# Kernel optimization log

Measured on AMD Instinct MI355X. Metric: run time of the kernel, lower is better.

Reference implementation:

```python
import jax, jax.numpy as jnp
import numpy as np
from math import pi

B, CIN, COUT, H, W, K, STRIDE, PAD = 4, 32, 64, 32, 32, 3, 1, 1


def setup_inputs() -> dict:
    key = jax.random.key(0)
    k1, k2, k3 = jax.random.split(key, 3)
    x = jax.random.normal(k1, (B, CIN, H, W), dtype=jnp.float32)
    probe = jax.random.uniform(k2, (1, CIN, COUT, 1, 1, K, K), dtype=jnp.float32, minval=-pi, maxval=pi)
    out_w = jax.random.uniform(k3, (1, CIN, COUT, 1, 1, K, K), dtype=jnp.float32, minval=-pi, maxval=pi)
    return {"x": x, "probe": probe, "out_w": out_w}


def _patches(x):
    # sliding-window gather, equivalent to x.unfold(2,K,S).unfold(3,K,S)
    p = jax.lax.conv_general_dilated_patches(
        x, filter_shape=(K, K), window_strides=(STRIDE, STRIDE),
        padding=[(PAD, PAD), (PAD, PAD)])  # (B, CIN*K*K, Ho, Wo), channel-major
    b, _, ho, wo = p.shape
    p = p.reshape(b, CIN, K, K, ho, wo)
    return jnp.transpose(p, (0, 1, 4, 5, 2, 3))  # (B, CIN, Ho, Wo, K, K)


def reference(x, probe, out_w):
    pat = _patches(x)[:, :, None]                 # (B, CIN, 1, Ho, Wo, K, K)
    act = jnp.cos(pat - probe) ** 3               # (B, CIN, COUT, Ho, Wo, K, K)
    cw = jnp.cos(out_w).reshape(CIN, COUT, K, K)  # squeeze broadcast dims
    sw = jnp.sin(out_w).reshape(CIN, COUT, K, K)
    out_x = jnp.einsum('cokl,bcohwkl->bohw', cw, act)
    out_y = jnp.einsum('cokl,bcohwkl->bohw', sw, act)
    return jnp.arctan2(out_y, out_x)              # (B, COUT, Ho, Wo)
```

## Files before the change

### kernel.cpp

```cpp
#include <hip/hip_runtime.h>
#include <math.h>


typedef _Float16 half8 __attribute__((ext_vector_type(8)));
typedef float floatx4 __attribute__((ext_vector_type(4)));

#define B_TAP_STRIDE (16 * 128 * 16)
#define B_VSTRIDE (9u * 16 * 128 * 16)

__global__ __launch_bounds__(256) void ring_prep_b(
    const float* __restrict__ probe, const float* __restrict__ outw,
    char* __restrict__ Bg) {
  int i = blockIdx.x * 256 + threadIdx.x;
  int q = i & 15;
  int n = (i >> 4) & 127;
  int tap = i >> 11;
  int o = n & 63;
  int xy = n >> 6;
  half8 hi, lo;
#pragma unroll
  for (int hf = 0; hf < 2; ++hf) {
    int c = q * 2 + hf;
    int idx = (c * 64 + o) * 9 + tap;
    float th = probe[idx];
    float wvv = outw[idx];
    float sth, cth, sw, cw;
    __sincosf(th, &sth, &cth);
    __sincosf(wvv, &sw, &cw);
    float c3 = cth * fmaf(4.0f * cth, cth, -3.0f);
    float s3 = sth * fmaf(-4.0f * sth, sth, 3.0f);
    float m = xy ? sw : cw;
    float v4[4] = {0.75f * m * cth, 0.75f * m * sth, 0.25f * m * c3,
                   0.25f * m * s3};
#pragma unroll
    for (int f = 0; f < 4; ++f) {
      _Float16 hv = (_Float16)v4[f];
      hi[hf * 4 + f] = hv;
      lo[hf * 4 + f] = (_Float16)((v4[f] - (float)hv) * 2048.0f);
    }
  }
  size_t off = (((size_t)tap * 16 + q) * 128 + n) * 16;
  *(half8*)(Bg + off) = hi;
  *(half8*)(Bg + off + B_VSTRIDE) = lo;
}

#define AL_OFF 26112

#define BLOAD(dst, base)                          \
  do {                                            \
    dst##0 = *(const half8*)((base));             \
    dst##1 = *(const half8*)((base) + 8192);      \
    dst##2 = *(const half8*)((base) + 16384);     \
    dst##3 = *(const half8*)((base) + 24576);     \
  } while (0)

__global__ __launch_bounds__(512, 2) void ring_mfma(
    const float* __restrict__ x, const char* __restrict__ Bg,
    float* __restrict__ out) {
  __shared__ __align__(16) char sA[52224];
  __shared__ float sEx[1024];

  int blk = blockIdx.x;
  int oh = blk & 1;
  int h = (blk >> 1) & 31;
  int b = blk >> 6;
  int tid = threadIdx.x;

  int lane = tid & 63;
  int wv = tid >> 6;
  int n16 = lane & 15;
  int quad = lane >> 4;
  int wt = wv >> 2;
  int xy = (wv >> 1) & 1;
  int og = wv & 1;

  int n_global = xy * 64 + oh * 32 + og * 16 + n16;
  const char* bLane = Bg + quad * 2048 + (size_t)n_global * 16;

  half8 BcH0, BcH1, BcH2, BcH3, BcL0, BcL1, BcL2, BcL3;
  half8 BnH0, BnH1, BnH2, BnH3, BnL0, BnL1, BnL2, BnL3;
  half8 BtH0, BtH1, BtH2, BtH3, BtL0, BtL1, BtL2, BtL3;
  BLOAD(BcH, bLane);
  BLOAD(BcL, bLane + B_VSTRIDE);
  BLOAD(BnH, bLane + B_TAP_STRIDE);
  BLOAD(BnL, bLane + B_TAP_STRIDE + B_VSTRIDE);

  {
    float xv0[4], xv1[4];
    bool act[4];
    int us[4];
#pragma unroll
    for (int it = 0; it < 4; ++it) {
      int u = tid + it * 512;
      us[it] = u;
      bool inr = u < 1632;
      int p = u & 15;
      int t = u >> 4;
      int colidx = t % 34;
      int r = t / 34;
      int q = p ^ (colidx & 7);
      int hs = h + r - 1;
      int wsx = colidx - 1;
      bool valid = inr && ((unsigned)hs < 32u) && ((unsigned)wsx < 32u);
      act[it] = inr;
      int base = ((b * 32) * 32 + ((unsigned)hs < 32u ? hs : 0)) * 32 +
                 ((unsigned)wsx < 32u ? wsx : 0);
      xv0[it] = valid ? x[base + (q * 2) * 1024] : 0.0f;
      xv1[it] = valid ? x[base + (q * 2 + 1) * 1024] : 0.0f;
    }
#pragma unroll
    for (int it = 0; it < 4; ++it) {
      if (!act[it]) continue;
      half8 hi, lo;
      float pv2[2] = {xv0[it], xv1[it]};
#pragma unroll
      for (int hf = 0; hf < 2; ++hf) {
        float s1, c1;
        __sincosf(pv2[hf], &s1, &c1);
        float c3 = c1 * fmaf(4.0f * c1, c1, -3.0f);
        float s3 = s1 * fmaf(-4.0f * s1, s1, 3.0f);
        float v4[4] = {c1, s1, c3, s3};
#pragma unroll
        for (int f = 0; f < 4; ++f) {
          _Float16 hv = (_Float16)v4[f];
          hi[hf * 4 + f] = hv;
          lo[hf * 4 + f] = (_Float16)((v4[f] - (float)hv) * 2048.0f);
        }
      }
      *(half8*)(sA + us[it] * 16) = hi;
      *(half8*)(sA + us[it] * 16 + AL_OFF) = lo;
    }
  }

  floatx4 acc0 = {0.f, 0.f, 0.f, 0.f};
  floatx4 acc1 = {0.f, 0.f, 0.f, 0.f};
  floatx4 acc2 = {0.f, 0.f, 0.f, 0.f};

  __syncthreads();

#pragma unroll
  for (int tap = 0; tap < 9; ++tap) {
    if (tap < 7) {
      const char* bt = bLane + (size_t)(tap + 2) * B_TAP_STRIDE;
      BLOAD(BtH, bt);
      BLOAD(BtL, bt + B_VSTRIDE);
    }

    int dk = tap / 3;
    int l = tap - dk * 3;
    int colidx = wt * 16 + n16 + l;
    int akey = colidx & 7;
    const char* aH = sA + (dk * 34 + colidx) * 256;
    const char* aL = aH + AL_OFF;

#pragma unroll
    for (int ks = 0; ks < 4; ++ks) {
      int pa = ((ks * 4 + quad) ^ akey) * 16;
      half8 Ah = *(const half8*)(aH + pa);
      half8 Al = *(const half8*)(aL + pa);
      half8 Bh = (ks == 0) ? BcH0 : (ks == 1) ? BcH1 : (ks == 2) ? BcH2 : BcH3;
      half8 Bl = (ks == 0) ? BcL0 : (ks == 1) ? BcL1 : (ks == 2) ? BcL2 : BcL3;
      acc0 = __builtin_amdgcn_mfma_f32_16x16x32_f16(Ah, Bh, acc0, 0, 0, 0);
      acc1 = __builtin_amdgcn_mfma_f32_16x16x32_f16(Al, Bh, acc1, 0, 0, 0);
      acc2 = __builtin_amdgcn_mfma_f32_16x16x32_f16(Ah, Bl, acc2, 0, 0, 0);
    }
    BcH0 = BnH0; BcH1 = BnH1; BcH2 = BnH2; BcH3 = BnH3;
    BcL0 = BnL0; BcL1 = BnL1; BcL2 = BnL2; BcL3 = BnL3;
    BnH0 = BtH0; BnH1 = BtH1; BnH2 = BtH2; BnH3 = BtH3;
    BnL0 = BtL0; BnL1 = BtL1; BnL2 = BtL2; BnL3 = BtL3;
  }

  floatx4 fin = acc0 + (acc1 + acc2) * (1.0f / 2048.0f);

  __syncthreads();
  if (xy == 1) {
#pragma unroll
    for (int r = 0; r < 4; ++r)
      sEx[((wt * 2 + og) * 16 + n16) * 16 + quad * 4 + r] = fin[r];
  }
  __syncthreads();
  if (xy == 0) {
    int o = oh * 32 + og * 16 + n16;
    float4 res;
    float* rp = (float*)&res;
#pragma unroll
    for (int r = 0; r < 4; ++r) {
      int m = quad * 4 + r;
      float ay = sEx[((wt * 2 + og) * 16 + n16) * 16 + m];
      rp[r] = atan2f(ay, fin[r]);
    }
    float* dst = out + (((size_t)(b * 64 + o) * 32 + h) * 32 + wt * 16 + quad * 4);
    *(float4*)dst = res;
  }
}

extern "C" void kernel_launch(void* const* d_in, const int* in_sizes, int n_in,
                              void* d_out, int out_size, void* d_ws, size_t ws_size,
                              hipStream_t stream) {
  const float* x = (const float*)d_in[0];
  const float* probe = (const float*)d_in[1];
  const float* outw = (const float*)d_in[2];
  char* Bg = (char*)d_ws;
  float* out = (float*)d_out;

  ring_prep_b<<<72, 256, 0, stream>>>(probe, outw, Bg);
  ring_mfma<<<256, 512, 0, stream>>>(x, Bg, out);
}
```

Before: 68.19 us.

## Fuse weight prep into main kernel with grid-wide atomic barrier

Folds the B-operand preparation kernel into the main MFMA kernel: each of 256 blocks prepares 72 entries, then all blocks meet at a spin barrier built on a global atomic counter, reset each call by a memset. The separate launch is gone, so prep and input staging overlap. The x staging is also remapped so consecutive threads read contiguous columns of one channel (coalesced) and write half4 pieces to shared memory. The grid barrier assumes all 256 blocks are resident at once; at 2 blocks/CU that holds on this GPU, but it adds a memset node and spin overhead.

```diff
diff --git a/kernel.cpp b/kernel.cpp
--- a/kernel.cpp
+++ b/kernel.cpp
@@ -3,59 +3,26 @@
 
 
 typedef _Float16 half8 __attribute__((ext_vector_type(8)));
+typedef _Float16 half4 __attribute__((ext_vector_type(4)));
 typedef float floatx4 __attribute__((ext_vector_type(4)));
 
 #define B_TAP_STRIDE (16 * 128 * 16)
 #define B_VSTRIDE (9u * 16 * 128 * 16)
-
-__global__ __launch_bounds__(256) void ring_prep_b(
-    const float* __restrict__ probe, const float* __restrict__ outw,
-    char* __restrict__ Bg) {
-  int i = blockIdx.x * 256 + threadIdx.x;
-  int q = i & 15;
-  int n = (i >> 4) & 127;
-  int tap = i >> 11;
-  int o = n & 63;
-  int xy = n >> 6;
-  half8 hi, lo;
-#pragma unroll
-  for (int hf = 0; hf < 2; ++hf) {
-    int c = q * 2 + hf;
-    int idx = (c * 64 + o) * 9 + tap;
-    float th = probe[idx];
-    float wvv = outw[idx];
-    float sth, cth, sw, cw;
-    __sincosf(th, &sth, &cth);
-    __sincosf(wvv, &sw, &cw);
-    float c3 = cth * fmaf(4.0f * cth, cth, -3.0f);
-    float s3 = sth * fmaf(-4.0f * sth, sth, 3.0f);
-    float m = xy ? sw : cw;
-    float v4[4] = {0.75f * m * cth, 0.75f * m * sth, 0.25f * m * c3,
-                   0.25f * m * s3};
-#pragma unroll
-    for (int f = 0; f < 4; ++f) {
-      _Float16 hv = (_Float16)v4[f];
-      hi[hf * 4 + f] = hv;
-      lo[hf * 4 + f] = (_Float16)((v4[f] - (float)hv) * 2048.0f);
-    }
-  }
-  size_t off = (((size_t)tap * 16 + q) * 128 + n) * 16;
-  *(half8*)(Bg + off) = hi;
-  *(half8*)(Bg + off + B_VSTRIDE) = lo;
-}
+#define FLAG_OFF (1u << 20)
 
 #define AL_OFF 26112
 
-#define BLOAD(dst, base)                          \
-  do {                                            \
-    dst##0 = *(const half8*)((base));             \
-    dst##1 = *(const half8*)((base) + 8192);      \
-    dst##2 = *(const half8*)((base) + 16384);     \
-    dst##3 = *(const half8*)((base) + 24576);     \
+#define BLOAD(dst, base)                     \
+  do {                                       \
+    dst##0 = *(const half8*)((base));        \
+    dst##1 = *(const half8*)((base) + 8192); \
+    dst##2 = *(const half8*)((base) + 16384);\
+    dst##3 = *(const half8*)((base) + 24576);\
   } while (0)
 
-__global__ __launch_bounds__(512, 2) void ring_mfma(
-    const float* __restrict__ x, const char* __restrict__ Bg,
+__global__ __launch_bounds__(512, 2) void ring_fused(
+    const float* __restrict__ x, const float* __restrict__ probe,
+    const float* __restrict__ outw, char* __restrict__ Bg,
     float* __restrict__ out) {
   __shared__ __align__(16) char sA[52224];
   __shared__ float sEx[1024];
@@ -65,6 +32,40 @@
   int h = (blk >> 1) & 31;
   int b = blk >> 6;
   int tid = threadIdx.x;
+
+  if (tid < 72) {
+    int i = blk * 72 + tid;
+    int q = i & 15;
+    int n = (i >> 4) & 127;
+    int tap = i >> 11;
+    int o = n & 63;
+    int xy = n >> 6;
+    half8 hi, lo;
+#pragma unroll
+    for (int hf = 0; hf < 2; ++hf) {
+      int c = q * 2 + hf;
+      int idx = (c * 64 + o) * 9 + tap;
+      float th = probe[idx];
+      float wvv = outw[idx];
+      float sth, cth, sw, cw;
+      __sincosf(th, &sth, &cth);
+      __sincosf(wvv, &sw, &cw);
+      float c3 = cth * fmaf(4.0f * cth, cth, -3.0f);
+      float s3 = sth * fmaf(-4.0f * sth, sth, 3.0f);
+      float m = xy ? sw : cw;
+      float v4[4] = {0.75f * m * cth, 0.75f * m * sth, 0.25f * m * c3,
+                     0.25f * m * s3};
+#pragma unroll
+      for (int f = 0; f < 4; ++f) {
+        _Float16 hv = (_Float16)v4[f];
+        hi[hf * 4 + f] = hv;
+        lo[hf * 4 + f] = (_Float16)((v4[f] - (float)hv) * 2048.0f);
+      }
+    }
+    size_t off = (((size_t)tap * 16 + q) * 128 + n) * 16;
+    *(half8*)(Bg + off) = hi;
+    *(half8*)(Bg + off + B_VSTRIDE) = lo;
+  }
 
   int lane = tid & 63;
   int wv = tid >> 6;
@@ -74,6 +75,64 @@
   int xy = (wv >> 1) & 1;
   int og = wv & 1;
 
+  {
+    float xv[7];
+#pragma unroll
+    for (int it = 0; it < 7; ++it) {
+      int u = tid + it * 512;
+      int colidx = u % 34;
+      int t = u / 34;
+      int c = t & 31;
+      int r = t >> 5;
+      int hs = h + r - 1;
+      int wsx = colidx - 1;
+      bool valid = (u < 3264) && ((unsigned)hs < 32u) && ((unsigned)wsx < 32u);
+      int xi = ((b * 32 + c) * 32 + ((unsigned)hs < 32u ? hs : 0)) * 32 +
+               ((unsigned)wsx < 32u ? wsx : 0);
+      xv[it] = valid ? x[xi] : 0.0f;
+    }
+#pragma unroll
+    for (int it = 0; it < 7; ++it) {
+      int u = tid + it * 512;
+      if (u < 3264) {
+        int colidx = u % 34;
+        int t = u / 34;
+        int c = t & 31;
+        int r = t >> 5;
+        int q = c >> 1;
+        int hf = c & 1;
+        int p = q ^ (colidx & 7);
+        float s1, c1;
+        __sincosf(xv[it], &s1, &c1);
+        float c3 = c1 * fmaf(4.0f * c1, c1, -3.0f);
+        float s3 = s1 * fmaf(-4.0f * s1, s1, 3.0f);
+        float v4[4] = {c1, s1, c3, s3};
+        half4 hi4, lo4;
+#pragma unroll
+        for (int f = 0; f < 4; ++f) {
+          _Float16 hv = (_Float16)v4[f];
+          hi4[f] = hv;
+          lo4[f] = (_Float16)((v4[f] - (float)hv) * 2048.0f);
+        }
+        int ub = ((r * 34 + colidx) * 16 + p) * 16 + hf * 8;
+        *(half4*)(sA + ub) = hi4;
+        *(half4*)(sA + ub + AL_OFF) = lo4;
+      }
+    }
+  }
+
+  __syncthreads();
+  unsigned int* flag = (unsigned int*)(Bg + FLAG_OFF);
+  if (tid == 0) {
+    __threadfence();
+    atomicAdd(flag, 1u);
+    while (atomicAdd(flag, 0u) < 256u) {
+      __builtin_amdgcn_s_sleep(8);
+    }
+    __threadfence();
+  }
+  __syncthreads();
+
   int n_global = xy * 64 + oh * 32 + og * 16 + n16;
   const char* bLane = Bg + quad * 2048 + (size_t)n_global * 16;
 
@@ -85,58 +144,9 @@
   BLOAD(BnH, bLane + B_TAP_STRIDE);
   BLOAD(BnL, bLane + B_TAP_STRIDE + B_VSTRIDE);
 
-  {
-    float xv0[4], xv1[4];
-    bool act[4];
-    int us[4];
-#pragma unroll
-    for (int it = 0; it < 4; ++it) {
-      int u = tid + it * 512;
-      us[it] = u;
-      bool inr = u < 1632;
-      int p = u & 15;
-      int t = u >> 4;
-      int colidx = t % 34;
-      int r = t / 34;
-      int q = p ^ (colidx & 7);
-      int hs = h + r - 1;
-      int wsx = colidx - 1;
-      bool valid = inr && ((unsigned)hs < 32u) && ((unsigned)wsx < 32u);
-      act[it] = inr;
-      int base = ((b * 32) * 32 + ((unsigned)hs < 32u ? hs : 0)) * 32 +
-                 ((unsigned)wsx < 32u ? wsx : 0);
-      xv0[it] = valid ? x[base + (q * 2) * 1024] : 0.0f;
-      xv1[it] = valid ? x[base + (q * 2 + 1) * 1024] : 0.0f;
-    }
-#pragma unroll
-    for (int it = 0; it < 4; ++it) {
-      if (!act[it]) continue;
-      half8 hi, lo;
-      float pv2[2] = {xv0[it], xv1[it]};
-#pragma unroll
-      for (int hf = 0; hf < 2; ++hf) {
-        float s1, c1;
-        __sincosf(pv2[hf], &s1, &c1);
-        float c3 = c1 * fmaf(4.0f * c1, c1, -3.0f);
-        float s3 = s1 * fmaf(-4.0f * s1, s1, 3.0f);
-        float v4[4] = {c1, s1, c3, s3};
-#pragma unroll
-        for (int f = 0; f < 4; ++f) {
-          _Float16 hv = (_Float16)v4[f];
-          hi[hf * 4 + f] = hv;
-          lo[hf * 4 + f] = (_Float16)((v4[f] - (float)hv) * 2048.0f);
-        }
-      }
-      *(half8*)(sA + us[it] * 16) = hi;
-      *(half8*)(sA + us[it] * 16 + AL_OFF) = lo;
-    }
-  }
-
   floatx4 acc0 = {0.f, 0.f, 0.f, 0.f};
   floatx4 acc1 = {0.f, 0.f, 0.f, 0.f};
   floatx4 acc2 = {0.f, 0.f, 0.f, 0.f};
-
-  __syncthreads();
 
 #pragma unroll
   for (int tap = 0; tap < 9; ++tap) {
@@ -203,6 +213,6 @@
   char* Bg = (char*)d_ws;
   float* out = (float*)d_out;
 
-  ring_prep_b<<<72, 256, 0, stream>>>(probe, outw, Bg);
-  ring_mfma<<<256, 512, 0, stream>>>(x, Bg, out);
+  hipMemsetAsync(Bg + FLAG_OFF, 0, 4, stream);
+  ring_fused<<<256, 512, 0, stream>>>(x, probe, outw, Bg, out);
 }
```

Result: slower. 80.06 us (+17.4%).
